# Optimization experiments

Measured on AMD Instinct MI355X. Metric: run time of the kernel, lower is better.

## Reference

```python
import jax, jax.numpy as jnp
import numpy as np

NC = 65536   # candidate centers across FPN levels (single image)
NP = 1024    # proposal boxes == points
D = 256      # points_feat_dim
C = 256      # in_channels (query/key dim)
START_LEVEL = 3
NEG = -1e30


def setup_inputs() -> dict:
    key = jax.random.key(0)
    ks = jax.random.split(key, 9)
    # centers: [y, x, size, stride]; stride in {8,16,32,64,128} -> lvl 0..4
    lvl = jax.random.randint(ks[0], (NC,), 0, 5)
    stride = (2.0 ** (lvl + START_LEVEL)).astype(jnp.float32)
    yx = jax.random.uniform(ks[1], (NC, 2), minval=0.0, maxval=1024.0)
    centers = jnp.concatenate([yx, stride[:, None], stride[:, None]], axis=1)
    # boxes: [x1, y1, x2, y2]
    x1y1 = jax.random.uniform(ks[2], (NP, 2), minval=0.0, maxval=900.0)
    wh = jax.random.uniform(ks[3], (NP, 2), minval=64.0, maxval=256.0)
    boxes = jnp.concatenate([x1y1, x1y1 + wh], axis=1)
    points_feat = jax.random.normal(ks[4], (NP, D), dtype=jnp.float32)
    box_feat = jax.random.normal(ks[5], (NC, D), dtype=jnp.float32)
    Wq = jax.random.normal(ks[6], (D, C), dtype=jnp.float32) / np.sqrt(D).astype(np.float32)
    bq = jnp.zeros((C,), dtype=jnp.float32)
    Wk = jax.random.normal(ks[7], (D, C), dtype=jnp.float32) / np.sqrt(D).astype(np.float32)
    bk = jnp.zeros((C,), dtype=jnp.float32)
    scales = 1.0 + 0.1 * jax.random.normal(ks[8], (5,), dtype=jnp.float32)
    return dict(points_feat=points_feat, box_feat=box_feat, centers=centers,
                boxes=boxes, Wq=Wq, bq=bq, Wk=Wk, bk=bk, scales=scales)


def reference(points_feat, box_feat, centers, boxes, Wq, bq, Wk, bk, scales):
    # geometry -> containment mask [NC, NP] (center c inside box p)
    coord = centers[:, :2] + jnp.floor_divide(centers[:, 2:3], 2.0)  # [NC,2]
    ys, xs = coord[:, 0], coord[:, 1]
    l = xs[:, None] - boxes[None, :, 0]
    t = ys[:, None] - boxes[None, :, 1]
    r = boxes[None, :, 2] - xs[:, None]
    b = boxes[None, :, 3] - ys[:, None]
    mask = jnp.minimum(jnp.minimum(l, t), jnp.minimum(r, b)) > 0     # [NC,NP]

    stride = centers[:, 3]
    lvl = (jnp.log2(stride) - START_LEVEL).astype(jnp.int32)         # [NC] in 0..4
    w = scales[lvl]                                                  # per-level scale

    query = points_feat @ Wq + bq                                    # [NP,C]
    keyf = (box_feat * w[:, None]) @ Wk + bk                         # [NC,C]

    sim = jnp.clip(keyf @ query.T, -50.0, 50.0)                      # [NC,NP]
    logits = jnp.where(mask, sim, NEG)
    attn = jax.nn.softmax(logits, axis=0)
    attn = jnp.where(mask, attn, 0.0)                                # zero out invalid
    merge = attn.T @ box_feat                                        # [NP,D]
    return points_feat + merge
```

## Files before the change

### kernel.cpp

```cpp
#include <hip/hip_runtime.h>

typedef unsigned short ushort_t;
typedef _Float16 half8 __attribute__((ext_vector_type(8)));
typedef short short8 __attribute__((ext_vector_type(8)));
typedef float floatx4 __attribute__((ext_vector_type(4)));

#define NCC 65536
#define NPP 1024
#define DD 256
#define NCHUNK 64
#define VROW 40
#define VTILE_B (256 * VROW * 2)
#define L2E 1.44269504f
#define CLIPL 72.134752f

static __device__ __forceinline__ ushort_t f2h_bits(float x) {
  _Float16 h = (_Float16)x;
  return __builtin_bit_cast(ushort_t, h);
}
static __device__ __forceinline__ ushort_t f2bf_bits(float x) {
  unsigned u = __builtin_bit_cast(unsigned, x);
  unsigned r = (u + 0x7FFFu + ((u >> 16) & 1u)) >> 16;
  return (ushort_t)r;
}
static __device__ __forceinline__ float bf2f(ushort_t b) {
  unsigned u = ((unsigned)b) << 16;
  return __builtin_bit_cast(float, u);
}
static __device__ __forceinline__ half8 cvt8(const float* p) {
  float4 a = *(const float4*)p, b = *(const float4*)(p + 4);
  half8 h;
  h[0] = (_Float16)a.x; h[1] = (_Float16)a.y; h[2] = (_Float16)a.z; h[3] = (_Float16)a.w;
  h[4] = (_Float16)b.x; h[5] = (_Float16)b.y; h[6] = (_Float16)b.z; h[7] = (_Float16)b.w;
  return h;
}
static __device__ __forceinline__ void dma16(const void* g, void* l) {
  __builtin_amdgcn_global_load_lds((const __attribute__((address_space(1))) unsigned int*)g,
                                   (__attribute__((address_space(3))) unsigned int*)l, 16, 0, 0);
}

__global__ __launch_bounds__(256) void mk_prep(const float* __restrict__ Wq,
                                               const float* __restrict__ Wk,
                                               const float* __restrict__ bq,
                                               const float* __restrict__ bk,
                                               ushort_t* __restrict__ MkF, float* __restrict__ tu,
                                               float* __restrict__ tv, float* __restrict__ s0v) {
  const int t = threadIdx.x;
  if (blockIdx.x == 16) {
    float su = 0.f, sv = 0.f;
    for (int j = 0; j < DD; j += 4) {
      float4 a = *(const float4*)&Wk[(size_t)t * DD + j];
      float4 b = *(const float4*)&bq[j];
      su += a.x * b.x + a.y * b.y + a.z * b.z + a.w * b.w;
      float4 c = *(const float4*)&Wq[(size_t)t * DD + j];
      float4 d = *(const float4*)&bk[j];
      sv += c.x * d.x + c.y * d.y + c.z * d.z + c.w * d.w;
    }
    tu[t] = su;
    tv[t] = sv;
    __shared__ float red[256];
    red[t] = bk[t] * bq[t];
    __syncthreads();
    for (int o = 128; o; o >>= 1) {
      if (t < o) red[t] += red[t + o];
      __syncthreads();
    }
    if (t == 0) s0v[0] = red[0];
    return;
  }
  const int m0 = ((int)blockIdx.x & 3) * 64, e0 = ((int)blockIdx.x >> 2) * 64;
  const int w = t >> 6, lane = t & 63, qd = lane >> 4, n = lane & 15;
  floatx4 acc[4] = {};
#pragma unroll
  for (int s = 0; s < 8; s++) {
    half8 af = cvt8(&Wk[(size_t)(m0 + w * 16 + n) * DD + s * 32 + qd * 8]);
#pragma unroll
    for (int nt = 0; nt < 4; ++nt) {
      half8 bf = cvt8(&Wq[(size_t)(e0 + nt * 16 + n) * DD + s * 32 + qd * 8]);
      acc[nt] = __builtin_amdgcn_mfma_f32_16x16x32_f16(af, bf, acc[nt], 0, 0, 0);
    }
  }
#pragma unroll
  for (int nt = 0; nt < 4; ++nt)
#pragma unroll
    for (int r = 0; r < 4; r++) {
      int mr = m0 + w * 16 + qd * 4 + r;
      int e = e0 + nt * 16 + n;
      size_t slot = ((size_t)(mr >> 4) * 8 + (e >> 5)) * 64 + ((e >> 3) & 3) * 16 + (mr & 15);
      MkF[slot * 8 + (e & 7)] = f2h_bits(acc[nt][r]);
    }
}

__global__ __launch_bounds__(256) void btgt_prep(
    const float* __restrict__ bf, const float* __restrict__ pf,
    const float* __restrict__ centers, const float* __restrict__ scales,
    const float* __restrict__ tu, const float* __restrict__ tv,
    const float* __restrict__ s0v, const ushort_t* __restrict__ MkF,
    ushort_t* __restrict__ bfR, ushort_t* __restrict__ vTb, float4* __restrict__ meta,
    ushort_t* __restrict__ Gt, float* __restrict__ gamma) {
  const int t = threadIdx.x;
  if (blockIdx.x >= (NCC / 32)) {
    const int p0 = ((int)blockIdx.x - NCC / 32) * 64;
    const int w = t >> 6, lane = t & 63, qd = lane >> 4, n = lane & 15;
    floatx4 acc[16] = {};
#pragma unroll
    for (int s = 0; s < 8; s++) {
      half8 af = cvt8(&pf[(size_t)(p0 + w * 16 + n) * DD + s * 32 + qd * 8]);
#pragma unroll
      for (int nt = 0; nt < 16; ++nt) {
        half8 bfr = __builtin_bit_cast(
            half8, *(const uint4*)&MkF[(((size_t)nt * 8 + s) * 64 + lane) * 8]);
        acc[nt] = __builtin_amdgcn_mfma_f32_16x16x32_f16(af, bfr, acc[nt], 0, 0, 0);
      }
    }
#pragma unroll
    for (int nt = 0; nt < 16; ++nt)
#pragma unroll
      for (int r = 0; r < 4; r++)
        Gt[(size_t)(p0 + w * 16 + qd * 4 + r) * DD + nt * 16 + n] = f2h_bits(acc[nt][r]);
    if (t < 64) {
      float s = s0v[0];
      for (int j = 0; j < DD; j += 4) {
        float4 a = *(const float4*)&pf[(size_t)(p0 + t) * DD + j];
        float4 b = *(const float4*)&tv[j];
        s += a.x * b.x + a.y * b.y + a.z * b.z + a.w * b.w;
      }
      gamma[p0 + t] = s * L2E - CLIPL;
    }
    return;
  }
  __shared__ float tu_s[256];
  __shared__ __align__(16) ushort_t lt[256][VROW];
  const int c0 = (int)blockIdx.x * 32;
  tu_s[t] = tu[t];
  __syncthreads();
  const int c = t >> 3, sub = t & 7;
  const int kc = ((c0 + c) & 3) | (((c0 + c) >> 1) & 4);
  float du = 0.f;
#pragma unroll
  for (int i = 0; i < 8; i++) {
    int f4 = sub + 8 * i;
    int d0 = f4 * 4;
    float4 v = *(const float4*)&bf[(size_t)(c0 + c) * DD + d0];
    du += v.x * tu_s[d0] + v.y * tu_s[d0 + 1] + v.z * tu_s[d0 + 2] + v.w * tu_s[d0 + 3];
    int l = f4 >> 1;
    int u = (l & ~7) | ((l & 7) ^ kc);
    ushort_t h0 = f2h_bits(v.x), h1 = f2h_bits(v.y), h2 = f2h_bits(v.z), h3 = f2h_bits(v.w);
    *(uint2*)&bfR[(size_t)(c0 + c) * DD + u * 8 + (d0 & 7)] =
        make_uint2((unsigned)h0 | ((unsigned)h1 << 16), (unsigned)h2 | ((unsigned)h3 << 16));
    lt[d0 + 0][c] = f2bf_bits(v.x);
    lt[d0 + 1][c] = f2bf_bits(v.y);
    lt[d0 + 2][c] = f2bf_bits(v.z);
    lt[d0 + 3][c] = f2bf_bits(v.w);
  }
  du += __shfl_xor(du, 1, 64);
  du += __shfl_xor(du, 2, 64);
  du += __shfl_xor(du, 4, 64);
  if (sub == 0) {
    const float4 ce = *(const float4*)&centers[(size_t)(c0 + c) * 4];
    int lvl = (int)(log2f(ce.w) + 0.5f) - 3;
    lvl = lvl < 0 ? 0 : (lvl > 4 ? 4 : lvl);
    float wsc = scales[lvl];
    float hf = floorf(ce.z * 0.5f);
    meta[c0 + c] = make_float4(wsc * L2E, wsc * du * L2E, ce.y + hf, ce.x + hf);
  }
  __syncthreads();
  char* dst = (char*)vTb + (size_t)blockIdx.x * VTILE_B + (size_t)t * (VROW * 2);
  const char* src = (const char*)&lt[t][0];
#pragma unroll
  for (int i = 0; i < 5; i++) *(uint4*)(dst + i * 16) = *(const uint4*)(src + i * 16);
}

template <bool PART>
__global__ __launch_bounds__(256, 2) void attn_kernel(
    const ushort_t* __restrict__ Gt, const float* __restrict__ gamma,
    const ushort_t* __restrict__ bfR, const ushort_t* __restrict__ vTb,
    const float4* __restrict__ meta, const float* __restrict__ boxes,
    void* __restrict__ acc_out, float* __restrict__ den_out) {
  __shared__ __align__(16) ushort_t lds_k[2][32 * 256];
  __shared__ __align__(16) ushort_t lds_v[2][256 * VROW];

  const int t = threadIdx.x;
  const int w = t >> 6, lane = t & 63, qd = lane >> 4, n = lane & 15;
  const int chunk = blockIdx.x;
  const int p0w = blockIdx.y * 128 + w * 32;
  const int cchunk = chunk * 1024;
  const int sw16 = (n & 7) * 16;

  half8 gfr[2][8];
  float4 bxv[2];
  float gam[2];
#pragma unroll
  for (int pt = 0; pt < 2; ++pt) {
    int p = p0w + pt * 16 + n;
#pragma unroll
    for (int s = 0; s < 8; s++)
      gfr[pt][s] = __builtin_bit_cast(half8, *(const uint4*)&Gt[(size_t)p * DD + s * 32 + qd * 8]);
    bxv[pt] = *(const float4*)&boxes[(size_t)p * 4];
    gam[pt] = gamma[p];
  }

  floatx4 macc[2][16] = {};
  float dsum0 = 0.f, dsum1 = 0.f;

  auto stage = [&](int it2, int b) {
    const char* ks = (const char*)bfR + (size_t)(cchunk + it2 * 32) * 512;
    char* kd = (char*)lds_k[b];
#pragma unroll
    for (int j = 0; j < 4; ++j) {
      int i = w * 4 + j;
      dma16(ks + i * 1024 + lane * 16, kd + i * 1024 + lane * 16);
    }
    const char* vs = (const char*)vTb + ((size_t)(cchunk >> 5) + it2) * VTILE_B;
    char* vd = (char*)lds_v[b];
#pragma unroll
    for (int j = 0; j < 5; ++j) {
      int i = w * 5 + j;
      dma16(vs + i * 1024 + lane * 16, vd + i * 1024 + lane * 16);
    }
  };

  stage(0, 0);

  for (int it = 0; it < 32; ++it) {
    const int buf = it & 1;
    const int cb = cchunk + it * 32;
    __syncthreads();
    if (it + 1 < 32) stage(it + 1, buf ^ 1);

    floatx4 at[2][2] = {};
#pragma unroll
    for (int t2 = 0; t2 < 2; ++t2) {
      const char* krow =
          (const char*)lds_k[buf] + ((((n & 12) << 1) + (n & 3) + 4 * t2) * 512);
#pragma unroll
      for (int s = 0; s < 8; s++) {
        half8 af = __builtin_bit_cast(half8, *(const uint4*)(krow + ((s * 64 + qd * 16) ^ sw16)));
        at[t2][0] = __builtin_amdgcn_mfma_f32_16x16x32_f16(af, gfr[0][s], at[t2][0], 0, 0, 0);
        at[t2][1] = __builtin_amdgcn_mfma_f32_16x16x32_f16(af, gfr[1][s], at[t2][1], 0, 0, 0);
      }
    }
    unsigned pk0[4], pk1[4];
#pragma unroll
    for (int t2 = 0; t2 < 2; ++t2) {
#pragma unroll
      for (int r = 0; r < 4; r++) {
        float4 mt = meta[cb + 8 * qd + 4 * t2 + r];
        {
          float mn = fminf(fminf(mt.z - bxv[0].x, mt.w - bxv[0].y),
                           fminf(bxv[0].z - mt.z, bxv[0].w - mt.w));
          float targ = fmaf(mt.x, at[t2][0][r], mt.y) + gam[0];
          float e = (mn > 0.f) ? exp2f(fminf(targ, 0.f)) : 0.f;
          dsum0 += e;
          unsigned b = (unsigned)f2bf_bits(e);
          unsigned idx = t2 * 2 + (r >> 1);
          if ((r & 1) == 0) pk0[idx] = b;
          else pk0[idx] |= b << 16;
        }
        {
          float mn = fminf(fminf(mt.z - bxv[1].x, mt.w - bxv[1].y),
                           fminf(bxv[1].z - mt.z, bxv[1].w - mt.w));
          float targ = fmaf(mt.x, at[t2][1][r], mt.y) + gam[1];
          float e = (mn > 0.f) ? exp2f(fminf(targ, 0.f)) : 0.f;
          dsum1 += e;
          unsigned b = (unsigned)f2bf_bits(e);
          unsigned idx = t2 * 2 + (r >> 1);
          if ((r & 1) == 0) pk1[idx] = b;
          else pk1[idx] |= b << 16;
        }
      }
    }
    uint4 u0, u1;
    u0.x = pk0[0]; u0.y = pk0[1]; u0.z = pk0[2]; u0.w = pk0[3];
    u1.x = pk1[0]; u1.y = pk1[1]; u1.z = pk1[2]; u1.w = pk1[3];
    short8 a20 = __builtin_bit_cast(short8, u0);
    short8 a21 = __builtin_bit_cast(short8, u1);
#pragma unroll
    for (int dt = 0; dt < 16; ++dt) {
      short8 b2 = __builtin_bit_cast(
          short8, *(const uint4*)&lds_v[buf][(dt * 16 + n) * VROW + qd * 8]);
      macc[0][dt] = __builtin_amdgcn_mfma_f32_16x16x32_bf16(a20, b2, macc[0][dt], 0, 0, 0);
      macc[1][dt] = __builtin_amdgcn_mfma_f32_16x16x32_bf16(a21, b2, macc[1][dt], 0, 0, 0);
    }
  }

  dsum0 += __shfl_xor(dsum0, 16, 64);
  dsum0 += __shfl_xor(dsum0, 32, 64);
  dsum1 += __shfl_xor(dsum1, 16, 64);
  dsum1 += __shfl_xor(dsum1, 32, 64);

  if (PART) {
    if (lane < 16) {
      den_out[(size_t)chunk * NPP + p0w + n] = dsum0;
      den_out[(size_t)chunk * NPP + p0w + 16 + n] = dsum1;
    }
    ushort_t* ab = (ushort_t*)acc_out + (size_t)chunk * NPP * DD;
#pragma unroll
    for (int pt = 0; pt < 2; ++pt)
#pragma unroll
      for (int dt = 0; dt < 16; ++dt)
#pragma unroll
        for (int r = 0; r < 4; r++)
          ab[(size_t)(p0w + pt * 16 + qd * 4 + r) * DD + dt * 16 + n] = f2bf_bits(macc[pt][dt][r]);
  } else {
    if (lane < 16) {
      atomicAdd(&den_out[p0w + n], dsum0);
      atomicAdd(&den_out[p0w + 16 + n], dsum1);
    }
    float* ab = (float*)acc_out;
#pragma unroll
    for (int pt = 0; pt < 2; ++pt)
#pragma unroll
      for (int dt = 0; dt < 16; ++dt)
#pragma unroll
        for (int r = 0; r < 4; r++)
          atomicAdd(&ab[(size_t)(p0w + pt * 16 + qd * 4 + r) * DD + dt * 16 + n],
                    macc[pt][dt][r]);
  }
}

__global__ __launch_bounds__(256) void reduce_finalize(const float* __restrict__ points_feat,
                                                       const ushort_t* __restrict__ acc_part,
                                                       const float* __restrict__ den_part,
                                                       float* __restrict__ out) {
  const int p = blockIdx.x, t = threadIdx.x;
  float s = 0.f;
#pragma unroll 4
  for (int c = 0; c < NCHUNK; ++c) s += bf2f(acc_part[((size_t)c * NPP + p) * DD + t]);
  float dn = den_part[(size_t)(t & 63) * NPP + p];
#pragma unroll
  for (int o = 1; o < 64; o <<= 1) dn += __shfl_xor(dn, o, 64);
  float m = (dn > 0.f) ? s / dn : 0.f;
  out[(size_t)p * DD + t] = points_feat[(size_t)p * DD + t] + m;
}

__global__ void finalize(const float* __restrict__ points_feat, const float* __restrict__ acc,
                         const float* __restrict__ den, float* __restrict__ out) {
  int p = blockIdx.x, d = threadIdx.x;
  float dn = den[p];
  float m = (dn > 0.f) ? acc[p * DD + d] / dn : 0.f;
  out[p * DD + d] = points_feat[p * DD + d] + m;
}

extern "C" void kernel_launch(void* const* d_in, const int* in_sizes, int n_in, void* d_out,
                              int out_size, void* d_ws, size_t ws_size, hipStream_t stream) {
  const float* points_feat = (const float*)d_in[0];
  const float* box_feat = (const float*)d_in[1];
  const float* centers = (const float*)d_in[2];
  const float* boxes = (const float*)d_in[3];
  const float* Wq = (const float*)d_in[4];
  const float* bq = (const float*)d_in[5];
  const float* Wk = (const float*)d_in[6];
  const float* bk = (const float*)d_in[7];
  const float* scales = (const float*)d_in[8];

  char* p = (char*)d_ws;
  ushort_t* ws_accP = (ushort_t*)p;  p += (size_t)NCHUNK * NPP * DD * 2;
  float* ws_den = (float*)p;         p += (size_t)NCHUNK * NPP * 4;
  ushort_t* ws_bfR = (ushort_t*)p;   p += (size_t)NCC * DD * 2;
  ushort_t* ws_vTb = (ushort_t*)p;   p += (size_t)(NCC / 32) * VTILE_B;
  ushort_t* ws_Gt = (ushort_t*)p;    p += (size_t)NPP * DD * 2;
  float4* ws_meta = (float4*)p;      p += (size_t)NCC * 16;
  float* ws_gamma = (float*)p;       p += (size_t)NPP * 4;
  size_t need_part = (size_t)(p - (char*)d_ws);

  if (ws_size >= need_part) {
    ushort_t* ws_Mk = ws_accP;
    float* ws_tu = (float*)(ws_Mk + (size_t)DD * DD);
    float* ws_tv = ws_tu + DD;
    float* ws_s0 = ws_tv + DD;

    mk_prep<<<17, 256, 0, stream>>>(Wq, Wk, bq, bk, ws_Mk, ws_tu, ws_tv, ws_s0);
    btgt_prep<<<NCC / 32 + 16, 256, 0, stream>>>(box_feat, points_feat, centers, scales, ws_tu,
                                                 ws_tv, ws_s0, ws_Mk, ws_bfR, ws_vTb, ws_meta,
                                                 ws_Gt, ws_gamma);
    attn_kernel<true><<<dim3(NCHUNK, 8), 256, 0, stream>>>(ws_Gt, ws_gamma, ws_bfR, ws_vTb,
                                                           ws_meta, boxes, ws_accP, ws_den);
    reduce_finalize<<<NPP, 256, 0, stream>>>(points_feat, ws_accP, ws_den, (float*)d_out);
  } else {
    char* q = (char*)d_ws;
    ushort_t* f_bfR = (ushort_t*)q;  q += (size_t)NCC * DD * 2;
    ushort_t* f_vTb = (ushort_t*)q;  q += (size_t)(NCC / 32) * VTILE_B;
    ushort_t* f_Gt = (ushort_t*)q;   q += (size_t)NPP * DD * 2;
    float4* f_meta = (float4*)q;     q += (size_t)NCC * 16;
    float* f_gamma = (float*)q;      q += (size_t)NPP * 4;
    float* f_den = (float*)q;        q += (size_t)NPP * 4;
    float* f_acc = (float*)q;        q += (size_t)NPP * DD * 4;
    ushort_t* f_Mk = (ushort_t*)f_acc;
    float* f_tu = (float*)(f_Mk + (size_t)DD * DD);
    float* f_tv = f_tu + DD;
    float* f_s0 = f_tv + DD;

    mk_prep<<<17, 256, 0, stream>>>(Wq, Wk, bq, bk, f_Mk, f_tu, f_tv, f_s0);
    btgt_prep<<<NCC / 32 + 16, 256, 0, stream>>>(box_feat, points_feat, centers, scales, f_tu,
                                                 f_tv, f_s0, f_Mk, f_bfR, f_vTb, f_meta, f_Gt,
                                                 f_gamma);
    hipMemsetAsync(f_den, 0, ((size_t)NPP * DD + NPP) * sizeof(float), stream);
    attn_kernel<false><<<dim3(NCHUNK, 8), 256, 0, stream>>>(f_Gt, f_gamma, f_bfR, f_vTb, f_meta,
                                                            boxes, f_acc, f_den);
    finalize<<<NPP, DD, 0, stream>>>(points_feat, f_acc, f_den, (float*)d_out);
  }
}
```

Baseline: 307.4 us.

## Shrink V tile padding, stage meta via LDS DMA, coalesce bfR writes

The transposed V tile row pitch drops from 40 to 36 elements, so each tile moves less data and the stage needs 18 DMA chunks instead of 20. V fragments are now read as two 8-byte LDS loads to fit the smaller pitch. Per-candidate meta is DMA'd into a double-buffered LDS array alongside K and V, replacing per-lane global float4 loads in the softmax loop. The prep kernel stages the swizzled fp16 key rows in LDS and writes them out as coalesced 16-byte stores. The costs are extra LDS instructions and a possible change in bank-conflict behaviour from the new pitch.

```diff
diff --git a/kernel.cpp b/kernel.cpp
--- a/kernel.cpp
+++ b/kernel.cpp
@@ -9,7 +9,7 @@
 #define NPP 1024
 #define DD 256
 #define NCHUNK 64
-#define VROW 40
+#define VROW 36
 #define VTILE_B (256 * VROW * 2)
 #define L2E 1.44269504f
 #define CLIPL 72.134752f
@@ -37,6 +37,11 @@
 static __device__ __forceinline__ void dma16(const void* g, void* l) {
   __builtin_amdgcn_global_load_lds((const __attribute__((address_space(1))) unsigned int*)g,
                                    (__attribute__((address_space(3))) unsigned int*)l, 16, 0, 0);
+}
+static __device__ __forceinline__ short8 mk_s8(uint2 lo, uint2 hi) {
+  uint4 u;
+  u.x = lo.x; u.y = lo.y; u.z = hi.x; u.w = hi.y;
+  return __builtin_bit_cast(short8, u);
 }
 
 __global__ __launch_bounds__(256) void mk_prep(const float* __restrict__ Wq,
@@ -131,6 +136,7 @@
   }
   __shared__ float tu_s[256];
   __shared__ __align__(16) ushort_t lt[256][VROW];
+  __shared__ __align__(16) ushort_t lds_r[32][256];
   const int c0 = (int)blockIdx.x * 32;
   tu_s[t] = tu[t];
   __syncthreads();
@@ -146,7 +152,7 @@
     int l = f4 >> 1;
     int u = (l & ~7) | ((l & 7) ^ kc);
     ushort_t h0 = f2h_bits(v.x), h1 = f2h_bits(v.y), h2 = f2h_bits(v.z), h3 = f2h_bits(v.w);
-    *(uint2*)&bfR[(size_t)(c0 + c) * DD + u * 8 + (d0 & 7)] =
+    *(uint2*)&lds_r[c][u * 8 + (d0 & 7)] =
         make_uint2((unsigned)h0 | ((unsigned)h1 << 16), (unsigned)h2 | ((unsigned)h3 << 16));
     lt[d0 + 0][c] = f2bf_bits(v.x);
     lt[d0 + 1][c] = f2bf_bits(v.y);
@@ -165,10 +171,17 @@
     meta[c0 + c] = make_float4(wsc * L2E, wsc * du * L2E, ce.y + hf, ce.x + hf);
   }
   __syncthreads();
+  {
+    int row = t >> 3, ch = t & 7;
+    const uint4* src = (const uint4*)&lds_r[row][ch * 32];
+    uint4* dst = (uint4*)&bfR[(size_t)(c0 + row) * DD + ch * 32];
+#pragma unroll
+    for (int i = 0; i < 4; i++) dst[i] = src[i];
+  }
   char* dst = (char*)vTb + (size_t)blockIdx.x * VTILE_B + (size_t)t * (VROW * 2);
   const char* src = (const char*)&lt[t][0];
 #pragma unroll
-  for (int i = 0; i < 5; i++) *(uint4*)(dst + i * 16) = *(const uint4*)(src + i * 16);
+  for (int i = 0; i < 9; i++) *(uint2*)(dst + i * 8) = *(const uint2*)(src + i * 8);
 }
 
 template <bool PART>
@@ -179,6 +192,7 @@
     void* __restrict__ acc_out, float* __restrict__ den_out) {
   __shared__ __align__(16) ushort_t lds_k[2][32 * 256];
   __shared__ __align__(16) ushort_t lds_v[2][256 * VROW];
+  __shared__ __align__(16) float4 lds_m[2][32];
 
   const int t = threadIdx.x;
   const int w = t >> 6, lane = t & 63, qd = lane >> 4, n = lane & 15;
@@ -214,17 +228,23 @@
     const char* vs = (const char*)vTb + ((size_t)(cchunk >> 5) + it2) * VTILE_B;
     char* vd = (char*)lds_v[b];
 #pragma unroll
-    for (int j = 0; j < 5; ++j) {
-      int i = w * 5 + j;
+    for (int j = 0; j < 4; ++j) {
+      int i = j * 4 + w;
       dma16(vs + i * 1024 + lane * 16, vd + i * 1024 + lane * 16);
     }
+    if (w < 2) {
+      int i = 16 + w;
+      dma16(vs + i * 1024 + lane * 16, vd + i * 1024 + lane * 16);
+    }
+    if (w == 0 && lane < 32)
+      dma16((const char*)meta + (size_t)(cchunk + it2 * 32) * 16 + lane * 16,
+            (char*)lds_m[b] + lane * 16);
   };
 
   stage(0, 0);
 
   for (int it = 0; it < 32; ++it) {
     const int buf = it & 1;
-    const int cb = cchunk + it * 32;
     __syncthreads();
     if (it + 1 < 32) stage(it + 1, buf ^ 1);
 
@@ -245,7 +265,7 @@
     for (int t2 = 0; t2 < 2; ++t2) {
 #pragma unroll
       for (int r = 0; r < 4; r++) {
-        float4 mt = meta[cb + 8 * qd + 4 * t2 + r];
+        float4 mt = lds_m[buf][8 * qd + 4 * t2 + r];
         {
           float mn = fminf(fminf(mt.z - bxv[0].x, mt.w - bxv[0].y),
                            fminf(bxv[0].z - mt.z, bxv[0].w - mt.w));
@@ -277,8 +297,8 @@
     short8 a21 = __builtin_bit_cast(short8, u1);
 #pragma unroll
     for (int dt = 0; dt < 16; ++dt) {
-      short8 b2 = __builtin_bit_cast(
-          short8, *(const uint4*)&lds_v[buf][(dt * 16 + n) * VROW + qd * 8]);
+      const ushort_t* vr = &lds_v[buf][(dt * 16 + n) * VROW + qd * 8];
+      short8 b2 = mk_s8(*(const uint2*)vr, *(const uint2*)(vr + 4));
       macc[0][dt] = __builtin_amdgcn_mfma_f32_16x16x32_bf16(a20, b2, macc[0][dt], 0, 0, 0);
       macc[1][dt] = __builtin_amdgcn_mfma_f32_16x16x32_bf16(a21, b2, macc[1][dt], 0, 0, 0);
     }
```

Measured after the change: 296.8 us. 1.04x faster.
